# Kernel tuning notes

Hardware: AMD Instinct MI355X
Metric: run time of the kernel (lower is better)

## Reference

```python
import jax, jax.numpy as jnp
import numpy as np

BITS = 8
CLIP_RATIO = 1.0
MAX_Q = 2 ** (BITS - 1) - 1  # 127
MIN_Q = -(MAX_Q + 1)         # -128


def setup_inputs() -> dict:
    key = jax.random.key(0)
    k1, k2, k3 = jax.random.split(key, 3)
    B, S, K, N = 4, 4096, 2048, 2048
    x = jax.random.normal(k1, (B, S, K), dtype=jnp.float32)
    # learned int8 weight [out_features, in_features] and per-row scale [out_features, 1]
    weight = jax.random.randint(k2, (N, K), MIN_Q, MAX_Q + 1, dtype=jnp.int32).astype(jnp.int8)
    weight_scale = jax.random.uniform(k3, (N, 1), dtype=jnp.float32, minval=1e-3, maxval=1e-2)
    return {"x": x, "weight": weight, "weight_scale": weight_scale}


def _quantize_sym(x):
    # per-token symmetric int8 quantization over the last dim
    mag = jnp.max(jnp.abs(x), axis=-1, keepdims=True) * CLIP_RATIO  # [B,S,1]
    scale = jnp.where(mag == 0, jnp.ones_like(mag), mag / MAX_Q)
    q = jnp.round(jnp.clip(x / scale, MIN_Q, MAX_Q)).astype(jnp.int8)
    return q, scale


def reference(x, weight, weight_scale):
    a, a_s = _quantize_sym(x)  # a: [B,S,K] int8, a_s: [B,S,1] f32
    res = jnp.einsum(
        'bsk,nk->bsn',
        a.astype(jnp.int32), weight.astype(jnp.int32),
    )  # [B,S,N] int32
    # dequantize: activation scale (per token) * weight scale (per out-channel)
    out = (res.astype(jnp.float32) * a_s * weight_scale.T).astype(x.dtype)
    return out
```

## Files before the change

kernel.cpp:

```cpp
#include <hip/hip_runtime.h>
#include <stdint.h>

#define M_DIM 16384
#define N_DIM 2048
#define K_DIM 2048

#define BM 256
#define BN 256
#define BK 64
#define NT (K_DIM / BK)
#define TILE_A_BYTES (BM * BK)
#define TILE_B_BYTES (BN * BK)
#define BUF_BYTES (TILE_A_BYTES + TILE_B_BYTES)
#define SMEM_BYTES (4 * BUF_BYTES)

typedef int v4i __attribute__((ext_vector_type(4)));

__global__ __launch_bounds__(256) void pack_w_kernel(const int* __restrict__ w32,
                                                     int8_t* __restrict__ w8) {
    const int i = (blockIdx.x * 256 + threadIdx.x) * 8;
    const int4 a = *reinterpret_cast<const int4*>(w32 + i);
    const int4 b = *reinterpret_cast<const int4*>(w32 + i + 4);
    uint32_t lo = (a.x & 255) | ((a.y & 255) << 8) | ((a.z & 255) << 16) | ((uint32_t)(a.w & 255) << 24);
    uint32_t hi = (b.x & 255) | ((b.y & 255) << 8) | ((b.z & 255) << 16) | ((uint32_t)(b.w & 255) << 24);
    int2 pk;
    pk.x = (int)lo;
    pk.y = (int)hi;
    *reinterpret_cast<int2*>(w8 + i) = pk;
}

__global__ __launch_bounds__(256) void quant_kernel(const float* __restrict__ x,
                                                    int8_t* __restrict__ q,
                                                    float* __restrict__ a_s) {
    const int lane = threadIdx.x & 63;
    const int wid = threadIdx.x >> 6;
    const int row = blockIdx.x * 4 + wid;

    const float4* xv = reinterpret_cast<const float4*>(x + (size_t)row * K_DIM);
    float4 v[8];
    #pragma unroll
    for (int j = 0; j < 8; ++j) v[j] = xv[lane + 64 * j];

    float m = 0.0f;
    #pragma unroll
    for (int j = 0; j < 8; ++j) {
        m = fmaxf(m, fmaxf(fmaxf(fabsf(v[j].x), fabsf(v[j].y)),
                           fmaxf(fabsf(v[j].z), fabsf(v[j].w))));
    }
    #pragma unroll
    for (int off = 32; off > 0; off >>= 1)
        m = fmaxf(m, __shfl_xor(m, off));
    const float mag = m;

    const float inv = (mag == 0.0f) ? 1.0f : (127.0f / mag);

    uint32_t* qo = reinterpret_cast<uint32_t*>(q + (size_t)row * K_DIM);
    #pragma unroll
    for (int j = 0; j < 8; ++j) {
        float e[4] = {v[j].x, v[j].y, v[j].z, v[j].w};
        uint32_t pk = 0;
        #pragma unroll
        for (int c = 0; c < 4; ++c) {
            float d = e[c] * inv;
            d = fminf(fmaxf(d, -128.0f), 127.0f);
            int qi = (int)rintf(d);
            pk |= ((uint32_t)(qi & 255)) << (8 * c);
        }
        qo[lane + 64 * j] = pk;
    }

    if (lane == 0) a_s[row] = (mag == 0.0f) ? 1.0f : (mag / 127.0f);
}

__global__ __launch_bounds__(512, 2) void gemm_i8_kernel(
    const int8_t* __restrict__ A,
    const int8_t* __restrict__ W,
    const float* __restrict__ a_s,
    const float* __restrict__ w_s,
    float* __restrict__ out)
{
    extern __shared__ int8_t smem[];

    const int t = threadIdx.x;
    const int lane = t & 63;
    const int wid = t >> 6;
    const int wr = wid >> 2;
    const int wc = wid & 3;

    const int bid = blockIdx.x;
    const int sbid = (bid & 7) * (gridDim.x >> 3) + (bid >> 3);
    const int bm = sbid >> 3;
    const int bn = sbid & 7;

    const int8_t* aSrc = A + (size_t)(bm * BM) * K_DIM;
    const int8_t* bSrc = W + (size_t)(bn * BN) * K_DIM;

    const int f0 = t, f1 = t + 512;
    const int r0 = f0 >> 2, u0 = f0 & 3;
    const int r1 = f1 >> 2, u1 = f1 & 3;
    const size_t gOff0 = (size_t)r0 * K_DIM + (size_t)((u0 ^ ((r0 >> 1) & 3)) << 4);
    const size_t gOff1 = (size_t)r1 * K_DIM + (size_t)((u1 ^ ((r1 >> 1) & 3)) << 4);

    #define STAGE_A(tile)                                                                   \
    do {                                                                                    \
        int8_t* base_ = smem + ((tile) & 3) * BUF_BYTES;                                    \
        const int k0_ = (tile) * BK;                                                        \
        __builtin_amdgcn_global_load_lds(                                                   \
            (const __attribute__((address_space(1))) void*)(aSrc + k0_ + gOff0),            \
            (__attribute__((address_space(3))) void*)(base_ + f0 * 16), 16, 0, 0);          \
        __builtin_amdgcn_global_load_lds(                                                   \
            (const __attribute__((address_space(1))) void*)(aSrc + k0_ + gOff1),            \
            (__attribute__((address_space(3))) void*)(base_ + f1 * 16), 16, 0, 0);          \
    } while (0)

    #define STAGE_B(tile)                                                                   \
    do {                                                                                    \
        int8_t* base_ = smem + ((tile) & 3) * BUF_BYTES + TILE_A_BYTES;                     \
        const int k0_ = (tile) * BK;                                                        \
        __builtin_amdgcn_global_load_lds(                                                   \
            (const __attribute__((address_space(1))) void*)(bSrc + k0_ + gOff0),            \
            (__attribute__((address_space(3))) void*)(base_ + f0 * 16), 16, 0, 0);          \
        __builtin_amdgcn_global_load_lds(                                                   \
            (const __attribute__((address_space(1))) void*)(bSrc + k0_ + gOff1),            \
            (__attribute__((address_space(3))) void*)(base_ + f1 * 16), 16, 0, 0);          \
    } while (0)

    const int frow = lane & 15;
    const int fc = lane >> 4;
    const int rA = wr * 128 + frow;
    const int rB = wc * 64 + frow;
    const int aOff = rA * 64 + ((((rA >> 1) & 3) ^ fc) << 4);
    const int bOff = rB * 64 + ((((rB >> 1) & 3) ^ fc) << 4);

    v4i acc[8][4] = {};

    STAGE_A(0); STAGE_B(0);
    STAGE_A(1); STAGE_B(1);
    STAGE_A(2); STAGE_B(2);
    asm volatile("s_waitcnt vmcnt(8)" ::: "memory");
    __builtin_amdgcn_s_barrier();
    asm volatile("" ::: "memory");

    for (int tt = 0; tt < NT; ++tt) {
        const int8_t* Ab = smem + (tt & 3) * BUF_BYTES;
        const int8_t* Bb = Ab + TILE_A_BYTES;
        const bool pf = (tt + 3 < NT);

        v4i af0[4], bf[4];
        #pragma unroll
        for (int mf = 0; mf < 4; ++mf)
            af0[mf] = *(const v4i*)(Ab + aOff + mf * 1024);
        #pragma unroll
        for (int nf = 0; nf < 4; ++nf)
            bf[nf] = *(const v4i*)(Bb + bOff + nf * 1024);
        if (pf) STAGE_A(tt + 3);

        asm volatile("" ::: "memory");
        __builtin_amdgcn_s_barrier();
        asm volatile("" ::: "memory");

        __builtin_amdgcn_s_setprio(1);
        #pragma unroll
        for (int mf = 0; mf < 4; ++mf)
            #pragma unroll
            for (int nf = 0; nf < 4; ++nf)
                acc[mf][nf] = __builtin_amdgcn_mfma_i32_16x16x64_i8(
                    af0[mf], bf[nf], acc[mf][nf], 0, 0, 0);
        __builtin_amdgcn_s_setprio(0);

        asm volatile("" ::: "memory");
        __builtin_amdgcn_s_barrier();
        asm volatile("" ::: "memory");

        v4i af1[4];
        #pragma unroll
        for (int mf = 0; mf < 4; ++mf)
            af1[mf] = *(const v4i*)(Ab + aOff + 4096 + mf * 1024);
        if (pf) STAGE_B(tt + 3);

        if (tt < NT - 1) {
            if (tt < NT - 3)      asm volatile("s_waitcnt vmcnt(8)" ::: "memory");
            else if (tt < NT - 2) asm volatile("s_waitcnt vmcnt(4)" ::: "memory");
            else                  asm volatile("s_waitcnt vmcnt(0)" ::: "memory");
        }
        __builtin_amdgcn_s_barrier();
        asm volatile("" ::: "memory");

        __builtin_amdgcn_s_setprio(1);
        #pragma unroll
        for (int mf = 0; mf < 4; ++mf)
            #pragma unroll
            for (int nf = 0; nf < 4; ++nf)
                acc[mf + 4][nf] = __builtin_amdgcn_mfma_i32_16x16x64_i8(
                    af1[mf], bf[nf], acc[mf + 4][nf], 0, 0, 0);
        __builtin_amdgcn_s_setprio(0);

        asm volatile("" ::: "memory");
        __builtin_amdgcn_s_barrier();
        asm volatile("" ::: "memory");
    }
    #undef STAGE_A
    #undef STAGE_B

    const int row0 = bm * BM + wr * 128;
    const int col0 = bn * BN + wc * 64;
    #pragma unroll
    for (int mf = 0; mf < 8; ++mf) {
        const int rbase = row0 + mf * 16 + (lane >> 4) * 4;
        #pragma unroll
        for (int nf = 0; nf < 4; ++nf) {
            const int c = col0 + nf * 16 + (lane & 15);
            const float ws = w_s[c];
            #pragma unroll
            for (int j = 0; j < 4; ++j) {
                const int r = rbase + j;
                out[(size_t)r * N_DIM + c] = ((float)acc[mf][nf][j] * a_s[r]) * ws;
            }
        }
    }
}

extern "C" void kernel_launch(void* const* d_in, const int* in_sizes, int n_in,
                              void* d_out, int out_size, void* d_ws, size_t ws_size,
                              hipStream_t stream) {
    const float* x = (const float*)d_in[0];
    const int* w32 = (const int*)d_in[1];
    const float* wscale = (const float*)d_in[2];
    float* out = (float*)d_out;

    int8_t* q = (int8_t*)d_ws;
    float* a_s = (float*)((char*)d_ws + (size_t)M_DIM * K_DIM);
    int8_t* w8 = (int8_t*)((char*)d_ws + (size_t)M_DIM * K_DIM + (size_t)M_DIM * 4);

    static int smem_set = 0;
    if (!smem_set) {
        hipFuncSetAttribute(reinterpret_cast<const void*>(&gemm_i8_kernel),
                            hipFuncAttributeMaxDynamicSharedMemorySize, SMEM_BYTES);
        smem_set = 1;
    }

    pack_w_kernel<<<(N_DIM * K_DIM) / (256 * 8), 256, 0, stream>>>(w32, w8);
    quant_kernel<<<M_DIM / 4, 256, 0, stream>>>(x, q, a_s);

    const int grid = (M_DIM / BM) * (N_DIM / BN);
    gemm_i8_kernel<<<grid, 512, SMEM_BYTES, stream>>>(q, w8, a_s, wscale, out);
}
```

Before: 311.5 us.

## Shrink GEMM tile to 256x128 with double-buffered static LDS and higher occupancy

Halves the N tile to 128, cuts the LDS pipeline from four buffers to two (static shared memory), and simplifies the main loop to one load phase and one MFMA phase per K-step with a single barrier. Each wave now holds a 64x64 accumulator instead of 128x64, and launch bounds ask for four blocks per CU, aiming for more resident waves to hide latency. The trade-off is lower arithmetic intensity per tile (more A reloads, since A is re-read for twice as many N tiles) and a shallower prefetch distance, with a full vmcnt(0) wait every iteration.

```diff
diff --git a/kernel.cpp b/kernel.cpp
--- a/kernel.cpp
+++ b/kernel.cpp
@@ -6,13 +6,12 @@
 #define K_DIM 2048
 
 #define BM 256
-#define BN 256
+#define BN 128
 #define BK 64
 #define NT (K_DIM / BK)
 #define TILE_A_BYTES (BM * BK)
 #define TILE_B_BYTES (BN * BK)
 #define BUF_BYTES (TILE_A_BYTES + TILE_B_BYTES)
-#define SMEM_BYTES (4 * BUF_BYTES)
 
 typedef int v4i __attribute__((ext_vector_type(4)));
 
@@ -72,92 +71,80 @@
     if (lane == 0) a_s[row] = (mag == 0.0f) ? 1.0f : (mag / 127.0f);
 }
 
-__global__ __launch_bounds__(512, 2) void gemm_i8_kernel(
+__global__ __launch_bounds__(512, 4) void gemm_i8_kernel(
     const int8_t* __restrict__ A,
     const int8_t* __restrict__ W,
     const float* __restrict__ a_s,
     const float* __restrict__ w_s,
     float* __restrict__ out)
 {
-    extern __shared__ int8_t smem[];
+    __shared__ __attribute__((aligned(16))) int8_t smem[2 * BUF_BYTES];
 
     const int t = threadIdx.x;
     const int lane = t & 63;
     const int wid = t >> 6;
-    const int wr = wid >> 2;
-    const int wc = wid & 3;
+    const int wr = wid >> 1;
+    const int wc = wid & 1;
 
     const int bid = blockIdx.x;
     const int sbid = (bid & 7) * (gridDim.x >> 3) + (bid >> 3);
-    const int bm = sbid >> 3;
-    const int bn = sbid & 7;
+    const int ntn = N_DIM / BN;
+    const int bm = sbid / ntn;
+    const int bn = sbid % ntn;
 
     const int8_t* aSrc = A + (size_t)(bm * BM) * K_DIM;
     const int8_t* bSrc = W + (size_t)(bn * BN) * K_DIM;
 
-    const int f0 = t, f1 = t + 512;
-    const int r0 = f0 >> 2, u0 = f0 & 3;
-    const int r1 = f1 >> 2, u1 = f1 & 3;
-    const size_t gOff0 = (size_t)r0 * K_DIM + (size_t)((u0 ^ ((r0 >> 1) & 3)) << 4);
-    const size_t gOff1 = (size_t)r1 * K_DIM + (size_t)((u1 ^ ((r1 >> 1) & 3)) << 4);
-
-    #define STAGE_A(tile)                                                                   \
+    const int fA0 = t, fA1 = t + 512, fB = t;
+    const int rA0 = fA0 >> 2, uA0 = fA0 & 3;
+    const int rA1 = fA1 >> 2, uA1 = fA1 & 3;
+    const int rBs = fB >> 2,  uBs = fB & 3;
+    const size_t gA0 = (size_t)rA0 * K_DIM + (size_t)((uA0 ^ ((rA0 >> 1) & 3)) << 4);
+    const size_t gA1 = (size_t)rA1 * K_DIM + (size_t)((uA1 ^ ((rA1 >> 1) & 3)) << 4);
+    const size_t gB0 = (size_t)rBs * K_DIM + (size_t)((uBs ^ ((rBs >> 1) & 3)) << 4);
+
+    #define STAGE(tile)                                                                     \
     do {                                                                                    \
-        int8_t* base_ = smem + ((tile) & 3) * BUF_BYTES;                                    \
+        int8_t* base_ = smem + ((tile) & 1) * BUF_BYTES;                                    \
         const int k0_ = (tile) * BK;                                                        \
         __builtin_amdgcn_global_load_lds(                                                   \
-            (const __attribute__((address_space(1))) void*)(aSrc + k0_ + gOff0),            \
-            (__attribute__((address_space(3))) void*)(base_ + f0 * 16), 16, 0, 0);          \
+            (const __attribute__((address_space(1))) void*)(aSrc + k0_ + gA0),              \
+            (__attribute__((address_space(3))) void*)(base_ + fA0 * 16), 16, 0, 0);         \
         __builtin_amdgcn_global_load_lds(                                                   \
-            (const __attribute__((address_space(1))) void*)(aSrc + k0_ + gOff1),            \
-            (__attribute__((address_space(3))) void*)(base_ + f1 * 16), 16, 0, 0);          \
-    } while (0)
-
-    #define STAGE_B(tile)                                                                   \
-    do {                                                                                    \
-        int8_t* base_ = smem + ((tile) & 3) * BUF_BYTES + TILE_A_BYTES;                     \
-        const int k0_ = (tile) * BK;                                                        \
+            (const __attribute__((address_space(1))) void*)(aSrc + k0_ + gA1),              \
+            (__attribute__((address_space(3))) void*)(base_ + fA1 * 16), 16, 0, 0);         \
         __builtin_amdgcn_global_load_lds(                                                   \
-            (const __attribute__((address_space(1))) void*)(bSrc + k0_ + gOff0),            \
-            (__attribute__((address_space(3))) void*)(base_ + f0 * 16), 16, 0, 0);          \
-        __builtin_amdgcn_global_load_lds(                                                   \
-            (const __attribute__((address_space(1))) void*)(bSrc + k0_ + gOff1),            \
-            (__attribute__((address_space(3))) void*)(base_ + f1 * 16), 16, 0, 0);          \
+            (const __attribute__((address_space(1))) void*)(bSrc + k0_ + gB0),              \
+            (__attribute__((address_space(3))) void*)(base_ + TILE_A_BYTES + fB * 16), 16, 0, 0); \
     } while (0)
 
     const int frow = lane & 15;
     const int fc = lane >> 4;
-    const int rA = wr * 128 + frow;
+    const int rA = wr * 64 + frow;
     const int rB = wc * 64 + frow;
     const int aOff = rA * 64 + ((((rA >> 1) & 3) ^ fc) << 4);
     const int bOff = rB * 64 + ((((rB >> 1) & 3) ^ fc) << 4);
 
-    v4i acc[8][4] = {};
-
-    STAGE_A(0); STAGE_B(0);
-    STAGE_A(1); STAGE_B(1);
-    STAGE_A(2); STAGE_B(2);
-    asm volatile("s_waitcnt vmcnt(8)" ::: "memory");
+    v4i acc[4][4] = {};
+
+    STAGE(0);
+    asm volatile("s_waitcnt vmcnt(0)" ::: "memory");
     __builtin_amdgcn_s_barrier();
     asm volatile("" ::: "memory");
 
     for (int tt = 0; tt < NT; ++tt) {
-        const int8_t* Ab = smem + (tt & 3) * BUF_BYTES;
+        if (tt + 1 < NT) STAGE(tt + 1);
+
+        const int8_t* Ab = smem + (tt & 1) * BUF_BYTES;
         const int8_t* Bb = Ab + TILE_A_BYTES;
-        const bool pf = (tt + 3 < NT);
-
-        v4i af0[4], bf[4];
+
+        v4i af[4], bf[4];
         #pragma unroll
         for (int mf = 0; mf < 4; ++mf)
-            af0[mf] = *(const v4i*)(Ab + aOff + mf * 1024);
+            af[mf] = *(const v4i*)(Ab + aOff + mf * 1024);
         #pragma unroll
         for (int nf = 0; nf < 4; ++nf)
             bf[nf] = *(const v4i*)(Bb + bOff + nf * 1024);
-        if (pf) STAGE_A(tt + 3);
-
-        asm volatile("" ::: "memory");
-        __builtin_amdgcn_s_barrier();
-        asm volatile("" ::: "memory");
 
         __builtin_amdgcn_s_setprio(1);
         #pragma unroll
@@ -165,47 +152,22 @@
             #pragma unroll
             for (int nf = 0; nf < 4; ++nf)
                 acc[mf][nf] = __builtin_amdgcn_mfma_i32_16x16x64_i8(
-                    af0[mf], bf[nf], acc[mf][nf], 0, 0, 0);
+                    af[mf], bf[nf], acc[mf][nf], 0, 0, 0);
         __builtin_amdgcn_s_setprio(0);
 
-        asm volatile("" ::: "memory");
-        __builtin_amdgcn_s_barrier();
-        asm volatile("" ::: "memory");
-
-        v4i af1[4];
-        #pragma unroll
-        for (int mf = 0; mf < 4; ++mf)
-            af1[mf] = *(const v4i*)(Ab + aOff + 4096 + mf * 1024);
-        if (pf) STAGE_B(tt + 3);
-
-        if (tt < NT - 1) {
-            if (tt < NT - 3)      asm volatile("s_waitcnt vmcnt(8)" ::: "memory");
-            else if (tt < NT - 2) asm volatile("s_waitcnt vmcnt(4)" ::: "memory");
-            else                  asm volatile("s_waitcnt vmcnt(0)" ::: "memory");
+        if (tt + 1 < NT) {
+            asm volatile("" ::: "memory");
+            asm volatile("s_waitcnt vmcnt(0)" ::: "memory");
+            __builtin_amdgcn_s_barrier();
+            asm volatile("" ::: "memory");
         }
-        __builtin_amdgcn_s_barrier();
-        asm volatile("" ::: "memory");
-
-        __builtin_amdgcn_s_setprio(1);
-        #pragma unroll
-        for (int mf = 0; mf < 4; ++mf)
-            #pragma unroll
-            for (int nf = 0; nf < 4; ++nf)
-                acc[mf + 4][nf] = __builtin_amdgcn_mfma_i32_16x16x64_i8(
-                    af1[mf], bf[nf], acc[mf + 4][nf], 0, 0, 0);
-        __builtin_amdgcn_s_setprio(0);
-
-        asm volatile("" ::: "memory");
-        __builtin_amdgcn_s_barrier();
-        asm volatile("" ::: "memory");
-    }
-    #undef STAGE_A
-    #undef STAGE_B
-
-    const int row0 = bm * BM + wr * 128;
+    }
+    #undef STAGE
+
+    const int row0 = bm * BM + wr * 64;
     const int col0 = bn * BN + wc * 64;
     #pragma unroll
-    for (int mf = 0; mf < 8; ++mf) {
+    for (int mf = 0; mf < 4; ++mf) {
         const int rbase = row0 + mf * 16 + (lane >> 4) * 4;
         #pragma unroll
         for (int nf = 0; nf < 4; ++nf) {
@@ -232,16 +194,9 @@
     float* a_s = (float*)((char*)d_ws + (size_t)M_DIM * K_DIM);
     int8_t* w8 = (int8_t*)((char*)d_ws + (size_t)M_DIM * K_DIM + (size_t)M_DIM * 4);
 
-    static int smem_set = 0;
-    if (!smem_set) {
-        hipFuncSetAttribute(reinterpret_cast<const void*>(&gemm_i8_kernel),
-                            hipFuncAttributeMaxDynamicSharedMemorySize, SMEM_BYTES);
-        smem_set = 1;
-    }
-
     pack_w_kernel<<<(N_DIM * K_DIM) / (256 * 8), 256, 0, stream>>>(w32, w8);
     quant_kernel<<<M_DIM / 4, 256, 0, stream>>>(x, q, a_s);
 
     const int grid = (M_DIM / BM) * (N_DIM / BN);
-    gemm_i8_kernel<<<grid, 512, SMEM_BYTES, stream>>>(q, w8, a_s, wscale, out);
-}
+    gemm_i8_kernel<<<grid, 512, 0, stream>>>(q, w8, a_s, wscale, out);
+}
```

New measurement: 306.2 us. About the same (-1.7%).

## Restructure int8 GEMM pipeline into half-tile staging with two tiles per iteration

Applied to the files above, without the earlier changes.

Splits each tile's global-to-LDS load into two halves (rows 0-127 and 128-255 of both A and B) that are issued across the phases of the loop. The main loop now processes two K-tiles per iteration with a prefetch distance of two tiles instead of three. It also adds explicit lgkmcnt(0) waits with scheduling barriers before each MFMA block. The aim is to spread memory traffic more evenly and tighten LDS synchronisation, at the cost of a shorter prefetch window and possible stalls on the added waits. The once-only guard around the shared-memory attribute call is removed, so that host API call now runs on every launch.

```diff
diff --git a/kernel.cpp b/kernel.cpp
--- a/kernel.cpp
+++ b/kernel.cpp
@@ -9,10 +9,10 @@
 #define BN 256
 #define BK 64
 #define NT (K_DIM / BK)
-#define TILE_A_BYTES (BM * BK)
-#define TILE_B_BYTES (BN * BK)
-#define BUF_BYTES (TILE_A_BYTES + TILE_B_BYTES)
-#define SMEM_BYTES (4 * BUF_BYTES)
+#define HALF_A 16384
+#define BUF_BYTES 32768
+#define NBUF 4
+#define SMEM_BYTES (NBUF * BUF_BYTES)
 
 typedef int v4i __attribute__((ext_vector_type(4)));
 
@@ -95,34 +95,21 @@
     const int8_t* aSrc = A + (size_t)(bm * BM) * K_DIM;
     const int8_t* bSrc = W + (size_t)(bn * BN) * K_DIM;
 
-    const int f0 = t, f1 = t + 512;
-    const int r0 = f0 >> 2, u0 = f0 & 3;
-    const int r1 = f1 >> 2, u1 = f1 & 3;
-    const size_t gOff0 = (size_t)r0 * K_DIM + (size_t)((u0 ^ ((r0 >> 1) & 3)) << 4);
-    const size_t gOff1 = (size_t)r1 * K_DIM + (size_t)((u1 ^ ((r1 >> 1) & 3)) << 4);
-
-    #define STAGE_A(tile)                                                                   \
+    const int rloc = t >> 2;
+    const int uch = t & 3;
+    const int swzu = ((uch ^ ((rloc >> 1) & 3)) << 4);
+    const size_t HROW = (size_t)128 * K_DIM;
+
+    #define STAGE_HALF(tl, h)                                                               \
     do {                                                                                    \
-        int8_t* base_ = smem + ((tile) & 3) * BUF_BYTES;                                    \
-        const int k0_ = (tile) * BK;                                                        \
+        int8_t* base_ = smem + ((tl) & 3) * BUF_BYTES + (h) * 8192;                         \
+        const size_t gr_ = (size_t)(tl) * BK + (h) * HROW + (size_t)rloc * K_DIM + swzu;    \
         __builtin_amdgcn_global_load_lds(                                                   \
-            (const __attribute__((address_space(1))) void*)(aSrc + k0_ + gOff0),            \
-            (__attribute__((address_space(3))) void*)(base_ + f0 * 16), 16, 0, 0);          \
+            (const __attribute__((address_space(1))) void*)(aSrc + gr_),                    \
+            (__attribute__((address_space(3))) void*)(base_ + t * 16), 16, 0, 0);           \
         __builtin_amdgcn_global_load_lds(                                                   \
-            (const __attribute__((address_space(1))) void*)(aSrc + k0_ + gOff1),            \
-            (__attribute__((address_space(3))) void*)(base_ + f1 * 16), 16, 0, 0);          \
-    } while (0)
-
-    #define STAGE_B(tile)                                                                   \
-    do {                                                                                    \
-        int8_t* base_ = smem + ((tile) & 3) * BUF_BYTES + TILE_A_BYTES;                     \
-        const int k0_ = (tile) * BK;                                                        \
-        __builtin_amdgcn_global_load_lds(                                                   \
-            (const __attribute__((address_space(1))) void*)(bSrc + k0_ + gOff0),            \
-            (__attribute__((address_space(3))) void*)(base_ + f0 * 16), 16, 0, 0);          \
-        __builtin_amdgcn_global_load_lds(                                                   \
-            (const __attribute__((address_space(1))) void*)(bSrc + k0_ + gOff1),            \
-            (__attribute__((address_space(3))) void*)(base_ + f1 * 16), 16, 0, 0);          \
+            (const __attribute__((address_space(1))) void*)(bSrc + gr_),                    \
+            (__attribute__((address_space(3))) void*)(base_ + HALF_A + t * 16), 16, 0, 0);  \
     } while (0)
 
     const int frow = lane & 15;
@@ -130,77 +117,95 @@
     const int rA = wr * 128 + frow;
     const int rB = wc * 64 + frow;
     const int aOff = rA * 64 + ((((rA >> 1) & 3) ^ fc) << 4);
-    const int bOff = rB * 64 + ((((rB >> 1) & 3) ^ fc) << 4);
+    const int bOff = HALF_A + rB * 64 + ((((rB >> 1) & 3) ^ fc) << 4);
+
+    #define LGKM0_FENCE()                                               \
+    do {                                                                \
+        asm volatile("s_waitcnt lgkmcnt(0)" ::: "memory");              \
+        __builtin_amdgcn_sched_barrier(0);                              \
+    } while (0)
 
     v4i acc[8][4] = {};
 
-    STAGE_A(0); STAGE_B(0);
-    STAGE_A(1); STAGE_B(1);
-    STAGE_A(2); STAGE_B(2);
-    asm volatile("s_waitcnt vmcnt(8)" ::: "memory");
+    STAGE_HALF(0, 0);
+    STAGE_HALF(0, 1);
+    STAGE_HALF(1, 0);
+    STAGE_HALF(1, 1);
+    asm volatile("s_waitcnt vmcnt(4)" ::: "memory");
     __builtin_amdgcn_s_barrier();
     asm volatile("" ::: "memory");
 
-    for (int tt = 0; tt < NT; ++tt) {
-        const int8_t* Ab = smem + (tt & 3) * BUF_BYTES;
-        const int8_t* Bb = Ab + TILE_A_BYTES;
-        const bool pf = (tt + 3 < NT);
-
-        v4i af0[4], bf[4];
-        #pragma unroll
-        for (int mf = 0; mf < 4; ++mf)
-            af0[mf] = *(const v4i*)(Ab + aOff + mf * 1024);
-        #pragma unroll
-        for (int nf = 0; nf < 4; ++nf)
-            bf[nf] = *(const v4i*)(Bb + bOff + nf * 1024);
-        if (pf) STAGE_A(tt + 3);
-
-        asm volatile("" ::: "memory");
+    for (int i = 0; i < NT / 2; ++i) {
+        const int t0 = 2 * i;
+        const bool pf = (t0 + 2 < NT);
+        const int8_t* B0 = smem + (t0 & 3) * BUF_BYTES;
+        const int8_t* B1 = smem + ((t0 + 1) & 3) * BUF_BYTES;
+
+        v4i af[4], bf[4];
+
+        #pragma unroll
+        for (int mf = 0; mf < 4; ++mf) af[mf] = *(const v4i*)(B0 + aOff + mf * 1024);
+        #pragma unroll
+        for (int nf = 0; nf < 4; ++nf) bf[nf] = *(const v4i*)(B0 + bOff + nf * 1024);
+        if (pf) STAGE_HALF(t0 + 2, 0);
         __builtin_amdgcn_s_barrier();
-        asm volatile("" ::: "memory");
-
-        __builtin_amdgcn_s_setprio(1);
-        #pragma unroll
-        for (int mf = 0; mf < 4; ++mf)
-            #pragma unroll
-            for (int nf = 0; nf < 4; ++nf)
-                acc[mf][nf] = __builtin_amdgcn_mfma_i32_16x16x64_i8(
-                    af0[mf], bf[nf], acc[mf][nf], 0, 0, 0);
-        __builtin_amdgcn_s_setprio(0);
-
-        asm volatile("" ::: "memory");
+        LGKM0_FENCE();
+        __builtin_amdgcn_s_setprio(1);
+        #pragma unroll
+        for (int mf = 0; mf < 4; ++mf)
+            #pragma unroll
+            for (int nf = 0; nf < 4; ++nf)
+                acc[mf][nf] = __builtin_amdgcn_mfma_i32_16x16x64_i8(af[mf], bf[nf], acc[mf][nf], 0, 0, 0);
+        __builtin_amdgcn_s_setprio(0);
+
+        #pragma unroll
+        for (int mf = 0; mf < 4; ++mf) af[mf] = *(const v4i*)(B0 + aOff + 4096 + mf * 1024);
+        if (pf) STAGE_HALF(t0 + 2, 1);
+        if (pf) asm volatile("s_waitcnt vmcnt(4)" ::: "memory");
+        else    asm volatile("s_waitcnt vmcnt(0)" ::: "memory");
         __builtin_amdgcn_s_barrier();
-        asm volatile("" ::: "memory");
-
-        v4i af1[4];
-        #pragma unroll
-        for (int mf = 0; mf < 4; ++mf)
-            af1[mf] = *(const v4i*)(Ab + aOff + 4096 + mf * 1024);
-        if (pf) STAGE_B(tt + 3);
-
-        if (tt < NT - 1) {
-            if (tt < NT - 3)      asm volatile("s_waitcnt vmcnt(8)" ::: "memory");
-            else if (tt < NT - 2) asm volatile("s_waitcnt vmcnt(4)" ::: "memory");
-            else                  asm volatile("s_waitcnt vmcnt(0)" ::: "memory");
+        LGKM0_FENCE();
+        __builtin_amdgcn_s_setprio(1);
+        #pragma unroll
+        for (int mf = 0; mf < 4; ++mf)
+            #pragma unroll
+            for (int nf = 0; nf < 4; ++nf)
+                acc[mf + 4][nf] = __builtin_amdgcn_mfma_i32_16x16x64_i8(af[mf], bf[nf], acc[mf + 4][nf], 0, 0, 0);
+        __builtin_amdgcn_s_setprio(0);
+
+        #pragma unroll
+        for (int mf = 0; mf < 4; ++mf) af[mf] = *(const v4i*)(B1 + aOff + mf * 1024);
+        #pragma unroll
+        for (int nf = 0; nf < 4; ++nf) bf[nf] = *(const v4i*)(B1 + bOff + nf * 1024);
+        if (pf) STAGE_HALF(t0 + 3, 0);
+        __builtin_amdgcn_s_barrier();
+        LGKM0_FENCE();
+        __builtin_amdgcn_s_setprio(1);
+        #pragma unroll
+        for (int mf = 0; mf < 4; ++mf)
+            #pragma unroll
+            for (int nf = 0; nf < 4; ++nf)
+                acc[mf][nf] = __builtin_amdgcn_mfma_i32_16x16x64_i8(af[mf], bf[nf], acc[mf][nf], 0, 0, 0);
+        __builtin_amdgcn_s_setprio(0);
+
+        #pragma unroll
+        for (int mf = 0; mf < 4; ++mf) af[mf] = *(const v4i*)(B1 + aOff + 4096 + mf * 1024);
+        if (pf) STAGE_HALF(t0 + 3, 1);
+        if (pf) {
+            asm volatile("s_waitcnt vmcnt(4)" ::: "memory");
+            __builtin_amdgcn_s_barrier();
         }
-        __builtin_amdgcn_s_barrier();
-        asm volatile("" ::: "memory");
-
-        __builtin_amdgcn_s_setprio(1);
-        #pragma unroll
-        for (int mf = 0; mf < 4; ++mf)
-            #pragma unroll
-            for (int nf = 0; nf < 4; ++nf)
-                acc[mf + 4][nf] = __builtin_amdgcn_mfma_i32_16x16x64_i8(
-                    af1[mf], bf[nf], acc[mf + 4][nf], 0, 0, 0);
-        __builtin_amdgcn_s_setprio(0);
-
-        asm volatile("" ::: "memory");
-        __builtin_amdgcn_s_barrier();
-        asm volatile("" ::: "memory");
-    }
-    #undef STAGE_A
-    #undef STAGE_B
+        LGKM0_FENCE();
+        __builtin_amdgcn_s_setprio(1);
+        #pragma unroll
+        for (int mf = 0; mf < 4; ++mf)
+            #pragma unroll
+            for (int nf = 0; nf < 4; ++nf)
+                acc[mf + 4][nf] = __builtin_amdgcn_mfma_i32_16x16x64_i8(af[mf], bf[nf], acc[mf + 4][nf], 0, 0, 0);
+        __builtin_amdgcn_s_setprio(0);
+    }
+    #undef STAGE_HALF
+    #undef LGKM0_FENCE
 
     const int row0 = bm * BM + wr * 128;
     const int col0 = bn * BN + wc * 64;
@@ -232,12 +237,8 @@
     float* a_s = (float*)((char*)d_ws + (size_t)M_DIM * K_DIM);
     int8_t* w8 = (int8_t*)((char*)d_ws + (size_t)M_DIM * K_DIM + (size_t)M_DIM * 4);
 
-    static int smem_set = 0;
-    if (!smem_set) {
-        hipFuncSetAttribute(reinterpret_cast<const void*>(&gemm_i8_kernel),
-                            hipFuncAttributeMaxDynamicSharedMemorySize, SMEM_BYTES);
-        smem_set = 1;
-    }
+    hipFuncSetAttribute(reinterpret_cast<const void*>(&gemm_i8_kernel),
+                        hipFuncAttributeMaxDynamicSharedMemorySize, SMEM_BYTES);
 
     pack_w_kernel<<<(N_DIM * K_DIM) / (256 * 8), 256, 0, stream>>>(w32, w8);
     quant_kernel<<<M_DIM / 4, 256, 0, stream>>>(x, q, a_s);
```

New measurement: 309.0 us. No clear change (-0.8%).
